# Optimization experiments

Measured on AMD Instinct MI355X. Metric: run time of the kernel, lower is better.

Reference implementation:

```python
import jax, jax.numpy as jnp
import numpy as np

H = 128          # hidden_channels == num_features for both node types
L = 3            # num_layers
E_TYPES = 3      # (a->a), (a->b), (b->a)
N = 200000       # nodes per type
E = 600000       # edges per edge type
G = 64           # graphs in batch
C = 10           # num_classes
BN_EPS = 1e-5


def setup_inputs() -> dict:
    key = jax.random.key(0)
    ks = jax.random.split(key, 16)
    x_a = jax.random.normal(ks[0], (N, H), dtype=jnp.float32)
    x_b = jax.random.normal(ks[1], (N, H), dtype=jnp.float32)
    ei_aa = jax.random.randint(ks[2], (2, E), 0, N, dtype=jnp.int32)
    ei_ab = jax.random.randint(ks[3], (2, E), 0, N, dtype=jnp.int32)
    ei_ba = jax.random.randint(ks[4], (2, E), 0, N, dtype=jnp.int32)
    batch_a = jnp.sort(jax.random.randint(ks[5], (N,), 0, G, dtype=jnp.int32))
    batch_b = jnp.sort(jax.random.randint(ks[6], (N,), 0, G, dtype=jnp.int32))
    s = 1.0 / np.sqrt(H)
    # GraphConv params per (layer, edge_type): lin_rel (weight+bias), lin_root (no bias)
    Wrel = jax.random.uniform(ks[7], (L, E_TYPES, H, H), jnp.float32, -s, s)
    brel = jax.random.uniform(ks[8], (L, E_TYPES, H), jnp.float32, -s, s)
    Wroot = jax.random.uniform(ks[9], (L, E_TYPES, H, H), jnp.float32, -s, s)
    # BatchNorm affine params per node type (0='a', 1='b')
    bn_gamma = jnp.ones((2, H), jnp.float32)
    bn_beta = jnp.zeros((2, H), jnp.float32)
    lin_W = jax.random.uniform(ks[10], (C, H), jnp.float32, -s, s)
    lin_b = jax.random.uniform(ks[11], (C,), jnp.float32, -s, s)
    return {"x_a": x_a, "x_b": x_b, "Wrel": Wrel, "brel": brel, "Wroot": Wroot,
            "bn_gamma": bn_gamma, "bn_beta": bn_beta, "lin_W": lin_W, "lin_b": lin_b,
            "ei_aa": ei_aa, "ei_ab": ei_ab, "ei_ba": ei_ba,
            "batch_a": batch_a, "batch_b": batch_b}


def _graph_conv(x_src, x_dst, ei, W_rel, b_rel, W_root):
    # PyG GraphConv (aggr='add'): out = lin_rel(sum_{j in N(i)} x_j) + lin_root(x_i)
    agg = jax.ops.segment_sum(x_src[ei[0]], ei[1], num_segments=x_dst.shape[0])
    return agg @ W_rel.T + b_rel + x_dst @ W_root.T


def _bn(x, gamma, beta):
    # BatchNorm in training mode: batch statistics (biased variance)
    mu = x.mean(axis=0)
    var = x.var(axis=0)
    return gamma * (x - mu) * jax.lax.rsqrt(var + BN_EPS) + beta


def reference(x_a, x_b, Wrel, brel, Wroot, bn_gamma, bn_beta, lin_W, lin_b,
              ei_aa, ei_ab, ei_ba, batch_a, batch_b):
    for l in range(L):
        # HeteroConv sums contributions per destination node type
        out_a = (_graph_conv(x_a, x_a, ei_aa, Wrel[l, 0], brel[l, 0], Wroot[l, 0]) +
                 _graph_conv(x_b, x_a, ei_ba, Wrel[l, 2], brel[l, 2], Wroot[l, 2]))
        out_b = _graph_conv(x_a, x_b, ei_ab, Wrel[l, 1], brel[l, 1], Wroot[l, 1])
        x_a = _bn(jax.nn.relu(out_a), bn_gamma[0], bn_beta[0])
        x_b = _bn(jax.nn.relu(out_b), bn_gamma[1], bn_beta[1])
    # global mean pool over concatenated node types
    feats = jnp.concatenate([x_a, x_b], axis=0)
    batch = jnp.concatenate([batch_a, batch_b], axis=0)
    sums = jax.ops.segment_sum(feats, batch, num_segments=G)
    counts = jax.ops.segment_sum(jnp.ones((feats.shape[0],), feats.dtype), batch, num_segments=G)
    pooled = sums / jnp.maximum(counts, 1.0)[:, None]
    return pooled @ lin_W.T + lin_b
```

## Files before the change

### kernel.cpp

```cpp
#include <hip/hip_runtime.h>
#include <hip/hip_bf16.h>

#define HF 128

typedef unsigned int uint32;
typedef unsigned short ushort16;
typedef float f32x4 __attribute__((ext_vector_type(4)));
typedef __bf16 bf16x8 __attribute__((ext_vector_type(8)));

__device__ __forceinline__ float bflo(uint32 u) { return __uint_as_float(u << 16); }
__device__ __forceinline__ float bfhi(uint32 u) { return __uint_as_float(u & 0xffff0000u); }
__device__ __forceinline__ ushort16 f2bf(float f) {
  uint32 u = __float_as_uint(f);
  return (ushort16)((u + 0x7fffu + ((u >> 16) & 1u)) >> 16);
}
__device__ __forceinline__ uint32 pack2(float lo, float hi) {
  return (uint32)f2bf(lo) | ((uint32)f2bf(hi) << 16);
}

__global__ void diag_k(float* __restrict__ out, int n, float val) {
  int i = blockIdx.x * 256 + threadIdx.x;
  if (i < n) out[i] = val;
}

__global__ __launch_bounds__(256) void setup_k(
    const float* __restrict__ xa, const float* __restrict__ xb,
    uint32* __restrict__ XA0, uint32* __restrict__ XA1, uint32* __restrict__ XB,
    int n4a, int n4b,
    int* __restrict__ cs, size_t capA, size_t capB, size_t capC, int vA, int vB,
    float* __restrict__ pool, int poolN4,
    size_t dummyA, size_t dummyB,
    int CA, int CB, int CI, int PZ) {
  int b = blockIdx.x, t = threadIdx.x;
  if (b < CA) {
    int i = b * 256 + t;
    if (i < n4a) {
      float4 v = ((const float4*)xa)[i];
      uint2 p; p.x = pack2(v.x, v.y); p.y = pack2(v.z, v.w);
      ((uint2*)XA0)[i] = p;
    }
    return;
  }
  b -= CA;
  if (b < CB) {
    int i = b * 256 + t;
    if (i < n4b) {
      float4 v = ((const float4*)xb)[i];
      uint2 p; p.x = pack2(v.x, v.y); p.y = pack2(v.z, v.w);
      ((uint2*)XB)[i] = p;
    }
    return;
  }
  b -= CB;
  if (b < CI) {
    size_t i = ((size_t)b * 256 + t) * 4;
    size_t tot = capA + capB + capC;
    if (i < tot) {
      int v = (i < capA + capB) ? vA : vB;
      int4 w = make_int4(v, v, v, v);
      *(int4*)&cs[i] = w;
    }
    return;
  }
  b -= CI;
  if (b < PZ) {
    int i = b * 256 + t;
    if (i < poolN4) ((float4*)pool)[i] = make_float4(0.f, 0.f, 0.f, 0.f);
    return;
  }
  if (t < 64) XA0[dummyA + t] = 0;
  else if (t < 128) XA1[dummyA + (t - 64)] = 0;
  else if (t < 192) XB[dummyB + (t - 128)] = 0;
}

__global__ void count3_k(const int* __restrict__ eA, int EA, int* __restrict__ rA,
                         const int* __restrict__ eB, int EB, int* __restrict__ rB,
                         const int* __restrict__ eC, int EC, int* __restrict__ rC,
                         int B0, int B1) {
  int b = blockIdx.x;
  const int* ei; int E; int* rp;
  if (b < B0)            { ei = eA; E = EA; rp = rA; }
  else if (b < B0 + B1)  { ei = eB; E = EB; rp = rB; b -= B0; }
  else                   { ei = eC; E = EC; rp = rC; b -= B0 + B1; }
  int e = b * 256 + threadIdx.x;
  if (e < E) atomicAdd(&rp[ei[E + e]], 1);
}

__device__ __forceinline__ int pad4(int c) { return (c + 3) & ~3; }

__device__ __forceinline__ void scan1_body(const int* __restrict__ rp, int N,
                                           int* __restrict__ bsum, int b, int t) {
  int i = b * 1024 + t * 4;
  int s = 0;
  if (i + 3 < N) {
    int4 v = *(const int4*)&rp[i];
    s = pad4(v.x) + pad4(v.y) + pad4(v.z) + pad4(v.w);
  } else {
    for (int j = 0; j < 4; ++j) if (i + j < N) s += pad4(rp[i + j]);
  }
  __shared__ int sd[256];
  sd[t] = s;
  __syncthreads();
  for (int o = 128; o > 0; o >>= 1) {
    if (t < o) sd[t] += sd[t + o];
    __syncthreads();
  }
  if (t == 0) bsum[b] = sd[0];
}

__global__ __launch_bounds__(256) void scan1x3_k(
    const int* __restrict__ rA, int NA, int* __restrict__ bA,
    const int* __restrict__ rB, int NB, int* __restrict__ bB,
    const int* __restrict__ rC, int NC, int* __restrict__ bC, int nbA, int nbB) {
  int b = blockIdx.x;
  if (b < nbA)            scan1_body(rA, NA, bA, b, threadIdx.x);
  else if (b < nbA + nbB) scan1_body(rB, NB, bB, b - nbA, threadIdx.x);
  else                    scan1_body(rC, NC, bC, b - nbA - nbB, threadIdx.x);
}

__global__ __launch_bounds__(1024) void scan2x3_k(int* __restrict__ bA, int nbA,
                                                  int* __restrict__ bB, int nbB,
                                                  int* __restrict__ bC, int nbC) {
  int* bsum = (blockIdx.x == 0) ? bA : (blockIdx.x == 1) ? bB : bC;
  int nb    = (blockIdx.x == 0) ? nbA : (blockIdx.x == 1) ? nbB : nbC;
  __shared__ int sd[1024];
  int t = threadIdx.x;
  int v = (t < nb) ? bsum[t] : 0;
  sd[t] = v;
  __syncthreads();
  for (int o = 1; o < 1024; o <<= 1) {
    int x = (t >= o) ? sd[t - o] : 0;
    __syncthreads();
    sd[t] += x;
    __syncthreads();
  }
  if (t < nb) bsum[t] = sd[t] - v;
}

__device__ __forceinline__ void scan3_body(int* __restrict__ rp, int* __restrict__ cur,
                                           int* __restrict__ deg,
                                           const int* __restrict__ bsum, int N,
                                           int b, int t) {
  int i = b * 1024 + t * 4;
  int c[4];
  #pragma unroll
  for (int j = 0; j < 4; ++j) c[j] = (i + j < N) ? rp[i + j] : 0;
  int tsum = pad4(c[0]) + pad4(c[1]) + pad4(c[2]) + pad4(c[3]);
  __shared__ int sd[256];
  sd[t] = tsum;
  __syncthreads();
  for (int o = 1; o < 256; o <<= 1) {
    int x = (t >= o) ? sd[t - o] : 0;
    __syncthreads();
    sd[t] += x;
    __syncthreads();
  }
  int off = bsum[b] + sd[t] - tsum;
  int p = off;
  #pragma unroll
  for (int j = 0; j < 4; ++j) {
    if (i + j < N) { rp[i + j] = p; cur[i + j] = p; deg[i + j] = c[j]; }
    p += pad4(c[j]);
  }
  if (i < N && N <= i + 4) rp[N] = off + tsum;
}

__global__ __launch_bounds__(256) void scan3x3_k(
    int* __restrict__ rA, int* __restrict__ cA, int* __restrict__ dA,
    const int* __restrict__ bA, int NA,
    int* __restrict__ rB, int* __restrict__ cB, int* __restrict__ dB,
    const int* __restrict__ bB, int NB,
    int* __restrict__ rC, int* __restrict__ cC, int* __restrict__ dC,
    const int* __restrict__ bC, int NC,
    int nbA, int nbB) {
  int b = blockIdx.x;
  if (b < nbA)            scan3_body(rA, cA, dA, bA, NA, b, threadIdx.x);
  else if (b < nbA + nbB) scan3_body(rB, cB, dB, bB, NB, b - nbA, threadIdx.x);
  else                    scan3_body(rC, cC, dC, bC, NC, b - nbA - nbB, threadIdx.x);
}

#define FILL_P 4
__global__ __launch_bounds__(256) void fill3p_k(
    const int* __restrict__ eA, int EA, int* __restrict__ cuA, int* __restrict__ csA,
    const int* __restrict__ eB, int EB, int* __restrict__ cuB, int* __restrict__ csB,
    const int* __restrict__ eC, int EC, int* __restrict__ cuC, int* __restrict__ csC,
    int NA, int NBn, int B0, int B1, int Btot) {
  int pass = blockIdx.x / Btot;
  int b = blockIdx.x % Btot;
  const int* ei; int E; int* cur; int* cs; int N;
  if (b < B0)           { ei = eA; E = EA; cur = cuA; cs = csA; N = NA; }
  else if (b < B0 + B1) { ei = eB; E = EB; cur = cuB; cs = csB; N = NBn; b -= B0; }
  else                  { ei = eC; E = EC; cur = cuC; cs = csC; N = NA; b -= B0 + B1; }
  int e = b * 256 + threadIdx.x;
  if (e >= E) return;
  int dst = ei[E + e];
  int lo = (int)(((long long)pass * N) / FILL_P);
  int hi = (int)(((long long)(pass + 1) * N) / FILL_P);
  if (dst < lo || dst >= hi) return;
  int pos = atomicAdd(&cur[dst], 1);
  cs[pos] = ei[e];
}

__global__ __launch_bounds__(128) void prep2_k(
    const float* __restrict__ Wrel_l, const float* __restrict__ Wroot_l,
    const float* __restrict__ brel_l,
    const float* __restrict__ gamma, const float* __restrict__ beta,
    const float* __restrict__ statsPrev, float* __restrict__ statsNext,
    float nA, float nB, int first,
    ushort16* __restrict__ BWa, ushort16* __restrict__ BWb,
    float* __restrict__ uvec) {
  __shared__ float red[128];
  int n = blockIdx.x, k = threadIdx.x;
  float scA, shA, scB, shB;
  if (first) {
    scA = 1.f; shA = 0.f; scB = 1.f; shB = 0.f;
  } else {
    float sA = 0.f, qA = 0.f, sB = 0.f, qB = 0.f;
    for (int st = 0; st < 64; ++st) {
      sA += statsPrev[st * 128 + k];
      qA += statsPrev[8192 + st * 128 + k];
      sB += statsPrev[16384 + st * 128 + k];
      qB += statsPrev[24576 + st * 128 + k];
    }
    float mA = sA / nA, vA = qA / nA - mA * mA;
    float rA = rsqrtf(vA + 1e-5f);
    scA = gamma[k] * rA; shA = beta[k] - mA * scA;
    float mB = sB / nB, vB = qB / nB - mB * mB;
    float rB = rsqrtf(vB + 1e-5f);
    scB = gamma[128 + k] * rB; shB = beta[128 + k] - mB * scB;
  }
  if (n < 64) {
    float4 z = make_float4(0.f, 0.f, 0.f, 0.f);
    *(float4*)&statsNext[n * 512 + k * 4] = z;
  }
  float w0  = Wrel_l[n * HF + k];
  float w1  = Wrel_l[16384 + n * HF + k];
  float w2  = Wrel_l[32768 + n * HF + k];
  float wr1 = Wroot_l[16384 + n * HF + k];
  float wrc = Wroot_l[n * HF + k] + Wroot_l[32768 + n * HF + k];

  int ksl = k >> 5;
  int lane = (n & 15) + (((k >> 3) & 3) << 4);
  int j = k & 7;
  int nt = n >> 4;
  auto put = [&](ushort16* B, int ksb, float v) {
    B[((size_t)((ksb + ksl) * 8 + nt) * 64 + lane) * 8 + j] = f2bf(v);
  };
  put(BWa, 0, scA * w0);
  put(BWa, 4, scB * w2);
  put(BWa, 8, scA * wrc);
  put(BWb, 0, scA * w1);
  put(BWb, 4, scB * wr1);

  auto reduce = [&](float v) -> float {
    red[k] = v;
    __syncthreads();
    for (int s = 64; s > 0; s >>= 1) {
      if (k < s) red[k] += red[k + s];
      __syncthreads();
    }
    float r = red[0];
    __syncthreads();
    return r;
  };
  float r0 = reduce(shA * w0);
  float r1 = reduce(shB * w2);
  float r2 = reduce(shA * w1);
  float r3 = reduce(shA * wrc);
  float r4 = reduce(shB * wr1);
  if (k == 0) {
    uvec[n]       = r0;
    uvec[128 + n] = r1;
    uvec[256 + n] = r2;
    uvec[384 + n] = brel_l[n] + brel_l[256 + n] + r3;
    uvec[512 + n] = brel_l[128 + n] + r4;
  }
}

template <bool HAS2>
__global__ __launch_bounds__(256) void gg_k(
    const uint32* __restrict__ Xg1, const int* __restrict__ rp1, const int* __restrict__ cs1,
    const int* __restrict__ deg1,
    const uint32* __restrict__ Xg2, const int* __restrict__ rp2, const int* __restrict__ cs2,
    const int* __restrict__ deg2,
    const uint32* Xr,
    const bf16x8* __restrict__ BW,
    const float* __restrict__ u1, const float* __restrict__ u2,
    const float* __restrict__ bias,
    uint32* out,
    float* __restrict__ statS, float* __restrict__ statQ,
    int nRows) {
  constexpr int KS_G = HAS2 ? 8 : 4;
  __shared__ uint32 lds[4][1088];
  int tid = threadIdx.x, wid = tid >> 6, l = tid & 63;
  int R0 = blockIdx.x * 64 + wid * 16;
  uint32* L = &lds[wid][0];
  int row = l & 15, khi = l >> 4;
  int myRow = R0 + row;
  bool okRow = myRow < nRows;
  int rowIdx = okRow ? myRow : nRows;

  int e0a = 0, e1a = 0;
  if (okRow) { e0a = rp1[myRow]; e1a = rp1[myRow + 1]; }
  int e0b = 0, e1b = 0;
  if constexpr (HAS2) { if (okRow) { e0b = rp2[myRow]; e1b = rp2[myRow + 1]; } }
  bf16x8 rt[4];
  #pragma unroll
  for (int ks = 0; ks < 4; ++ks)
    rt[ks] = *(const bf16x8*)&Xr[(size_t)rowIdx * 64 + (ks * 4 + khi) * 4];
  int4 q1 = make_int4(0, 0, 0, 0), q2 = make_int4(0, 0, 0, 0);
  if (e0a < e1a) q1 = *(const int4*)&cs1[e0a];
  if constexpr (HAS2) { if (e0b < e1b) q2 = *(const int4*)&cs2[e0b]; }
  int rl0 = khi * 4;
  float dg1[4] = {0.f, 0.f, 0.f, 0.f}, dg2[4] = {0.f, 0.f, 0.f, 0.f};
  #pragma unroll
  for (int j = 0; j < 4; ++j) {
    int r = R0 + rl0 + j;
    if (r < nRows) {
      dg1[j] = (float)deg1[r];
      if constexpr (HAS2) dg2[j] = (float)deg2[r];
    }
  }

  float lo[16], hi[16];
  auto addv = [&](int base, uint4 v) {
    hi[base + 0] += __uint_as_float(v.x); lo[base + 0] += __uint_as_float(v.x << 16);
    hi[base + 1] += __uint_as_float(v.y); lo[base + 1] += __uint_as_float(v.y << 16);
    hi[base + 2] += __uint_as_float(v.z); lo[base + 2] += __uint_as_float(v.z << 16);
    hi[base + 3] += __uint_as_float(v.w); lo[base + 3] += __uint_as_float(v.w << 16);
  };
  auto run_tile = [&](const uint32* __restrict__ Xg, const int* __restrict__ cs,
                      int e0, int e1, int4 qinit) {
    #pragma unroll
    for (int i = 0; i < 16; ++i) { lo[i] = 0.f; hi[i] = 0.f; }
    if (e0 >= e1) return;
    int e = e0;
    int4 q = qinit;
    for (;;) {
      const uint32* p0 = &Xg[(size_t)q.x * 64 + khi * 4];
      const uint32* p1 = &Xg[(size_t)q.y * 64 + khi * 4];
      const uint32* p2 = &Xg[(size_t)q.z * 64 + khi * 4];
      const uint32* p3 = &Xg[(size_t)q.w * 64 + khi * 4];
      uint4 a0 = *(const uint4*)&p0[0];
      uint4 a1 = *(const uint4*)&p0[16];
      uint4 a2 = *(const uint4*)&p0[32];
      uint4 a3 = *(const uint4*)&p0[48];
      uint4 b0 = *(const uint4*)&p1[0];
      uint4 b1 = *(const uint4*)&p1[16];
      uint4 b2 = *(const uint4*)&p1[32];
      uint4 b3 = *(const uint4*)&p1[48];
      uint4 c0 = *(const uint4*)&p2[0];
      uint4 c1 = *(const uint4*)&p2[16];
      uint4 c2 = *(const uint4*)&p2[32];
      uint4 c3 = *(const uint4*)&p2[48];
      uint4 d0 = *(const uint4*)&p3[0];
      uint4 d1 = *(const uint4*)&p3[16];
      uint4 d2 = *(const uint4*)&p3[32];
      uint4 d3 = *(const uint4*)&p3[48];
      int en = e + 4;
      bool more = en < e1;
      int4 qn = q;
      if (more) qn = *(const int4*)&cs[en];
      addv(0, a0); addv(4, a1); addv(8, a2); addv(12, a3);
      addv(0, b0); addv(4, b1); addv(8, b2); addv(12, b3);
      addv(0, c0); addv(4, c1); addv(8, c2); addv(12, c3);
      addv(0, d0); addv(4, d1); addv(8, d2); addv(12, d3);
      if (!more) break;
      e = en; q = qn;
    }
  };
  auto to_frag = [&](int ks) -> bf16x8 {
    bf16x8 a;
    #pragma unroll
    for (int j = 0; j < 4; ++j) {
      a[2 * j]     = (__bf16)lo[ks * 4 + j];
      a[2 * j + 1] = (__bf16)hi[ks * 4 + j];
    }
    return a;
  };

  run_tile(Xg1, cs1, e0a, e1a, q1);
  bf16x8 af1[4];
  #pragma unroll
  for (int ks = 0; ks < 4; ++ks) af1[ks] = to_frag(ks);

  bf16x8 af2[4];
  if constexpr (HAS2) {
    run_tile(Xg2, cs2, e0b, e1b, q2);
    #pragma unroll
    for (int ks = 0; ks < 4; ++ks) af2[ks] = to_frag(ks);
  }

  f32x4 acc[8] = {};
  const bf16x8* Bl = BW + l;
  #pragma unroll
  for (int ks = 0; ks < 4; ++ks) {
    #pragma unroll
    for (int nt = 0; nt < 8; ++nt) {
      bf16x8 b = Bl[(size_t)(ks * 8 + nt) * 64];
      acc[nt] = __builtin_amdgcn_mfma_f32_16x16x32_bf16(af1[ks], b, acc[nt], 0, 0, 0);
    }
  }
  if constexpr (HAS2) {
    #pragma unroll
    for (int ks = 0; ks < 4; ++ks) {
      #pragma unroll
      for (int nt = 0; nt < 8; ++nt) {
        bf16x8 b = Bl[(size_t)((4 + ks) * 8 + nt) * 64];
        acc[nt] = __builtin_amdgcn_mfma_f32_16x16x32_bf16(af2[ks], b, acc[nt], 0, 0, 0);
      }
    }
  }
  #pragma unroll
  for (int ks = 0; ks < 4; ++ks) {
    #pragma unroll
    for (int nt = 0; nt < 8; ++nt) {
      bf16x8 b = Bl[(size_t)((KS_G + ks) * 8 + nt) * 64];
      acc[nt] = __builtin_amdgcn_mfma_f32_16x16x32_bf16(rt[ks], b, acc[nt], 0, 0, 0);
    }
  }

  ushort16* P = (ushort16*)L;
  int c0 = l & 15;
  float ps[8], pq[8];
  #pragma unroll
  for (int nt = 0; nt < 8; ++nt) {
    int col = nt * 16 + c0;
    float bc = bias[col];
    float u1c = u1[col];
    float u2c = HAS2 ? u2[col] : 0.f;
    float s = 0.f, q = 0.f;
    #pragma unroll
    for (int j = 0; j < 4; ++j) {
      float v = acc[nt][j] + bc + dg1[j] * u1c;
      if constexpr (HAS2) v += dg2[j] * u2c;
      v = fmaxf(v, 0.f);
      if (R0 + rl0 + j < nRows) { s += v; q += v * v; }
      P[(rl0 + j) * 136 + col] = f2bf(v);
    }
    ps[nt] = s; pq[nt] = q;
  }

  #pragma unroll
  for (int rr = 0; rr < 4; ++rr) {
    int rloc = rr * 4 + khi;
    int grow = R0 + rloc;
    if (grow < nRows) {
      uint4 v = *(const uint4*)&P[rloc * 136 + c0 * 8];
      *(uint4*)&out[(size_t)grow * 64 + c0 * 4] = v;
    }
  }

  #pragma unroll
  for (int nt = 0; nt < 8; ++nt) {
    ps[nt] += __shfl_xor(ps[nt], 16); ps[nt] += __shfl_xor(ps[nt], 32);
    pq[nt] += __shfl_xor(pq[nt], 16); pq[nt] += __shfl_xor(pq[nt], 32);
  }
  if (l < 16) {
    float* S = statS + (size_t)(blockIdx.x & 63) * 128;
    float* Q = statQ + (size_t)(blockIdx.x & 63) * 128;
    #pragma unroll
    for (int nt = 0; nt < 8; ++nt) {
      unsafeAtomicAdd(&S[nt * 16 + l], ps[nt]);
      unsafeAtomicAdd(&Q[nt * 16 + l], pq[nt]);
    }
  }
}

__global__ void bn_fin_k(const float* __restrict__ stats, const float* __restrict__ gamma,
                         const float* __restrict__ beta, float* __restrict__ ss,
                         float nA, float nB) {
  int t = threadIdx.x;
  if (t >= 256) return;
  int type = t >> 7, f = t & 127;
  const float* S = stats + (size_t)type * 16384;
  const float* Q = S + 8192;
  float s = 0.f, q = 0.f;
  for (int st = 0; st < 64; ++st) { s += S[st * 128 + f]; q += Q[st * 128 + f]; }
  float nN = type ? nB : nA;
  float mean = s / nN;
  float var = q / nN - mean * mean;
  float rstd = rsqrtf(var + 1e-5f);
  float sc = gamma[type * HF + f] * rstd;
  float sh = beta[type * HF + f] - mean * sc;
  ss[type * 256 + f] = sc;
  ss[type * 256 + 128 + f] = sh;
}

__global__ __launch_bounds__(256) void pool_k(const uint32* __restrict__ x,
                                              const int* __restrict__ batch,
                                              const float* __restrict__ scale,
                                              const float* __restrict__ shift,
                                              float* __restrict__ pool, int nN) {
  int f2 = threadIdx.x & 31;
  int sub = threadIdx.x >> 5;
  int start = blockIdx.x * 1024;
  int end = min(start + 1024, nN);
  float4 sc = *(const float4*)&scale[f2 * 4];
  float4 sh = *(const float4*)&shift[f2 * 4];
  float a0 = 0.f, a1 = 0.f, a2 = 0.f, a3 = 0.f, cnt = 0.f;
  int cur = -1;
  for (int n = start + sub; n < end; n += 8) {
    int g = batch[n];
    if (g != cur) {
      if (cur >= 0) {
        float* bp = &pool[(size_t)cur * HF + f2 * 4];
        unsafeAtomicAdd(bp + 0, sc.x * a0 + cnt * sh.x);
        unsafeAtomicAdd(bp + 1, sc.y * a1 + cnt * sh.y);
        unsafeAtomicAdd(bp + 2, sc.z * a2 + cnt * sh.z);
        unsafeAtomicAdd(bp + 3, sc.w * a3 + cnt * sh.w);
      }
      a0 = a1 = a2 = a3 = 0.f; cnt = 0.f; cur = g;
    }
    uint2 v = *(const uint2*)&x[(size_t)n * 64 + f2 * 2];
    a0 += bflo(v.x); a1 += bfhi(v.x); a2 += bflo(v.y); a3 += bfhi(v.y);
    cnt += 1.f;
  }
  if (cur >= 0) {
    float* bp = &pool[(size_t)cur * HF + f2 * 4];
    unsafeAtomicAdd(bp + 0, sc.x * a0 + cnt * sh.x);
    unsafeAtomicAdd(bp + 1, sc.y * a1 + cnt * sh.y);
    unsafeAtomicAdd(bp + 2, sc.z * a2 + cnt * sh.z);
    unsafeAtomicAdd(bp + 3, sc.w * a3 + cnt * sh.w);
  }
}

__device__ inline int lowerb(const int* a, int n, int v) {
  int lo = 0, hi = n;
  while (lo < hi) { int m = (lo + hi) >> 1; if (a[m] < v) lo = m + 1; else hi = m; }
  return lo;
}

__global__ void final_k(const float* __restrict__ pool,
                        const int* __restrict__ ba, int nA,
                        const int* __restrict__ bb, int nB,
                        const float* __restrict__ linW, const float* __restrict__ linb,
                        float* __restrict__ out, int Cn) {
  int g = blockIdx.x;
  int lane = threadIdx.x;
  int c = (lowerb(ba, nA, g + 1) - lowerb(ba, nA, g)) +
          (lowerb(bb, nB, g + 1) - lowerb(bb, nB, g));
  float inv = 1.f / fmaxf((float)c, 1.f);
  float p0 = pool[(size_t)g * HF + lane] * inv;
  float p1 = pool[(size_t)g * HF + 64 + lane] * inv;
  for (int cc = 0; cc < Cn; ++cc) {
    float t = p0 * linW[cc * HF + lane] + p1 * linW[cc * HF + 64 + lane];
    for (int off = 32; off > 0; off >>= 1) t += __shfl_down(t, off);
    if (lane == 0) out[g * Cn + cc] = t + linb[cc];
  }
}

extern "C" void kernel_launch(void* const* d_in, const int* in_sizes, int n_in,
                              void* d_out, int out_size, void* d_ws, size_t ws_size,
                              hipStream_t stream) {
  const float* x_a   = (const float*)d_in[0];
  const float* x_b   = (const float*)d_in[1];
  const float* Wrel  = (const float*)d_in[2];
  const float* brel  = (const float*)d_in[3];
  const float* Wroot = (const float*)d_in[4];
  const float* bn_g  = (const float*)d_in[5];
  const float* bn_b  = (const float*)d_in[6];
  const float* lin_W = (const float*)d_in[7];
  const float* lin_b = (const float*)d_in[8];
  const int* ei_aa   = (const int*)d_in[9];
  const int* ei_ab   = (const int*)d_in[10];
  const int* ei_ba   = (const int*)d_in[11];
  const int* batch_a = (const int*)d_in[12];
  const int* batch_b = (const int*)d_in[13];

  int Na  = in_sizes[0] / HF;
  int Nb  = in_sizes[1] / HF;
  int Eaa = in_sizes[9] / 2;
  int Eab = in_sizes[10] / 2;
  int Eba = in_sizes[11] / 2;
  int Cn  = in_sizes[7] / HF;
  int Gn  = out_size / Cn;

  size_t NHa = (size_t)Na * HF, NHb = (size_t)Nb * HF;
  size_t capA = ((size_t)Eaa + 3 * (size_t)Na + 15) & ~(size_t)15;
  size_t capB = ((size_t)Eab + 3 * (size_t)Nb + 15) & ~(size_t)15;
  size_t capC = ((size_t)Eba + 3 * (size_t)Na + 15) & ~(size_t)15;

  char* base = (char*)d_ws;
  auto alignup = [](size_t x) { return (x + 255) & ~(size_t)255; };
  size_t off = 0;
  size_t oXA0 = off; off = alignup(off + (NHa + HF) * 2);
  size_t oXA1 = off; off = alignup(off + (NHa + HF) * 2);
  size_t oXB  = off; off = alignup(off + (NHb + HF) * 2);
  size_t oRP  = off; off = alignup(off + ((size_t)(Na + 1) + (Nb + 1) + (Na + 1)) * 4);
  size_t oCUR = off; off = alignup(off + ((size_t)Na + Nb + Na) * 4);
  size_t oDEG = off; off = alignup(off + ((size_t)Na + Nb + Na) * 4);
  size_t oCS  = off; off = alignup(off + (capA + capB + capC) * 4);
  size_t oBWA = off; off = alignup(off + (size_t)12 * 8 * 64 * 16);
  size_t oBWB = off; off = alignup(off + (size_t)8 * 8 * 64 * 16);
  size_t oUV  = off; off = alignup(off + 5 * 128 * 4);
  size_t oSS  = off; off = alignup(off + 512 * 4);
  size_t oST  = off; off = alignup(off + 65536 * 4);
  size_t oBS  = off; off = alignup(off + 3072 * 4);
  size_t oPOOL= off; off = alignup(off + (size_t)Gn * HF * 4);
  size_t need = off;

  if (ws_size < need) {
    diag_k<<<(out_size + 255) / 256, 256, 0, stream>>>(
        (float*)d_out, out_size, (float)((double)ws_size / 1048576.0));
    return;
  }

  uint32* XA0 = (uint32*)(base + oXA0);
  uint32* XA1 = (uint32*)(base + oXA1);
  uint32* XB  = (uint32*)(base + oXB);
  int* rp_aa = (int*)(base + oRP);
  int* rp_ab = rp_aa + (Na + 1);
  int* rp_ba = rp_ab + (Nb + 1);
  int* cur_aa = (int*)(base + oCUR);
  int* cur_ab = cur_aa + Na;
  int* cur_ba = cur_ab + Nb;
  int* deg_aa = (int*)(base + oDEG);
  int* deg_ab = deg_aa + Na;
  int* deg_ba = deg_ab + Nb;
  int* cs_aa = (int*)(base + oCS);
  int* cs_ab = cs_aa + capA;
  int* cs_ba = cs_ab + capB;
  ushort16* BWa = (ushort16*)(base + oBWA);
  ushort16* BWb = (ushort16*)(base + oBWB);
  float* uvec  = (float*)(base + oUV);
  float* ss    = (float*)(base + oSS);
  float* stats = (float*)(base + oST);
  int* bsum    = (int*)(base + oBS);
  float* pool  = (float*)(base + oPOOL);

  float* ss_a = ss;
  float* ss_b = ss + 256;
  float* uaa = uvec, *uba = uvec + 128, *uab = uvec + 256;
  float* bias_a = uvec + 384, *bias_b = uvec + 512;

  int n4a = (int)(NHa / 4), n4b = (int)(NHb / 4);
  int CA = (n4a + 255) / 256, CB = (n4b + 255) / 256;
  size_t capTot = capA + capB + capC;
  int CI = (int)((capTot / 4 + 255) / 256);
  int poolN4 = Gn * HF / 4;
  int PZ = (poolN4 + 255) / 256;
  setup_k<<<CA + CB + CI + PZ + 1, 256, 0, stream>>>(
      x_a, x_b, XA0, XA1, XB, n4a, n4b,
      cs_aa, capA, capB, capC, Na, Nb,
      pool, poolN4, NHa / 2, NHb / 2, CA, CB, CI, PZ);

  hipMemsetAsync(rp_aa, 0, ((size_t)(Na + 1) + (Nb + 1) + (Na + 1)) * 4, stream);
  int B0 = (Eaa + 255) / 256, B1 = (Eab + 255) / 256, B2 = (Eba + 255) / 256;
  count3_k<<<B0 + B1 + B2, 256, 0, stream>>>(ei_aa, Eaa, rp_aa, ei_ab, Eab, rp_ab,
                                             ei_ba, Eba, rp_ba, B0, B1);

  int nb_a = (Na + 1023) / 1024;
  int nb_b = (Nb + 1023) / 1024;
  scan1x3_k<<<nb_a + nb_b + nb_a, 256, 0, stream>>>(
      rp_aa, Na, bsum, rp_ab, Nb, bsum + 1024, rp_ba, Na, bsum + 2048, nb_a, nb_b);
  scan2x3_k<<<3, 1024, 0, stream>>>(bsum, nb_a, bsum + 1024, nb_b, bsum + 2048, nb_a);
  scan3x3_k<<<nb_a + nb_b + nb_a, 256, 0, stream>>>(
      rp_aa, cur_aa, deg_aa, bsum, Na,
      rp_ab, cur_ab, deg_ab, bsum + 1024, Nb,
      rp_ba, cur_ba, deg_ba, bsum + 2048, Na, nb_a, nb_b);

  int Btot = B0 + B1 + B2;
  fill3p_k<<<FILL_P * Btot, 256, 0, stream>>>(ei_aa, Eaa, cur_aa, cs_aa,
                                              ei_ab, Eab, cur_ab, cs_ab,
                                              ei_ba, Eba, cur_ba, cs_ba,
                                              Na, Nb, B0, B1, Btot);

  uint32* xa_cur = XA0;
  uint32* xa_nxt = XA1;
  for (int l = 0; l < 3; ++l) {
    const float* Wrel_l  = Wrel  + (size_t)l * 3 * 16384;
    const float* Wroot_l = Wroot + (size_t)l * 3 * 16384;
    const float* brel_l  = brel  + (size_t)l * 3 * HF;
    float* statsCur  = stats + (size_t)(l & 1) * 32768;
    float* statsPrev = stats + (size_t)((l + 1) & 1) * 32768;

    prep2_k<<<128, 128, 0, stream>>>(Wrel_l, Wroot_l, brel_l, bn_g, bn_b,
                                     statsPrev, statsCur, (float)Na, (float)Nb,
                                     (l == 0) ? 1 : 0, BWa, BWb, uvec);

    gg_k<true><<<(Na + 63) / 64, 256, 0, stream>>>(
        xa_cur, rp_aa, cs_aa, deg_aa, XB, rp_ba, cs_ba, deg_ba, xa_cur,
        (const bf16x8*)BWa, uaa, uba, bias_a, xa_nxt,
        statsCur, statsCur + 8192, Na);
    gg_k<false><<<(Nb + 63) / 64, 256, 0, stream>>>(
        xa_cur, rp_ab, cs_ab, deg_ab, nullptr, nullptr, nullptr, nullptr, XB,
        (const bf16x8*)BWb, uab, nullptr, bias_b, XB,
        statsCur + 16384, statsCur + 24576, Nb);

    uint32* t = xa_cur; xa_cur = xa_nxt; xa_nxt = t;
  }

  bn_fin_k<<<1, 256, 0, stream>>>(stats, bn_g, bn_b, ss, (float)Na, (float)Nb);

  pool_k<<<(Na + 1023) / 1024, 256, 0, stream>>>(xa_cur, batch_a, ss_a, ss_a + 128, pool, Na);
  pool_k<<<(Nb + 1023) / 1024, 256, 0, stream>>>(XB, batch_b, ss_b, ss_b + 128, pool, Nb);
  final_k<<<Gn, 64, 0, stream>>>(pool, batch_a, Na, batch_b, Nb,
                                 lin_W, lin_b, (float*)d_out, Cn);
}
```

Before: 969.4 us.

## Merge per-layer a/b GraphConv kernels into one launch with double-buffered XB

```diff
diff --git a/kernel.cpp b/kernel.cpp
--- a/kernel.cpp
+++ b/kernel.cpp
@@ -25,12 +25,14 @@
 
 __global__ __launch_bounds__(256) void setup_k(
     const float* __restrict__ xa, const float* __restrict__ xb,
-    uint32* __restrict__ XA0, uint32* __restrict__ XA1, uint32* __restrict__ XB,
+    uint32* __restrict__ XA0, uint32* __restrict__ XA1,
+    uint32* __restrict__ XB0, uint32* __restrict__ XB1,
     int n4a, int n4b,
     int* __restrict__ cs, size_t capA, size_t capB, size_t capC, int vA, int vB,
     float* __restrict__ pool, int poolN4,
+    int* __restrict__ rpz, int rpN4,
     size_t dummyA, size_t dummyB,
-    int CA, int CB, int CI, int PZ) {
+    int CA, int CB, int CI, int PZ, int RZ) {
   int b = blockIdx.x, t = threadIdx.x;
   if (b < CA) {
     int i = b * 256 + t;
@@ -47,7 +49,7 @@
     if (i < n4b) {
       float4 v = ((const float4*)xb)[i];
       uint2 p; p.x = pack2(v.x, v.y); p.y = pack2(v.z, v.w);
-      ((uint2*)XB)[i] = p;
+      ((uint2*)XB0)[i] = p;
     }
     return;
   }
@@ -68,9 +70,16 @@
     if (i < poolN4) ((float4*)pool)[i] = make_float4(0.f, 0.f, 0.f, 0.f);
     return;
   }
+  b -= PZ;
+  if (b < RZ) {
+    int i = b * 256 + t;
+    if (i < rpN4) ((int4*)rpz)[i] = make_int4(0, 0, 0, 0);
+    return;
+  }
   if (t < 64) XA0[dummyA + t] = 0;
   else if (t < 128) XA1[dummyA + (t - 64)] = 0;
-  else if (t < 192) XB[dummyB + (t - 128)] = 0;
+  else if (t < 192) XB0[dummyB + (t - 128)] = 0;
+  else XB1[dummyB + (t - 192)] = 0;
 }
 
 __global__ void count3_k(const int* __restrict__ eA, int EA, int* __restrict__ rA,
@@ -278,7 +287,8 @@
 }
 
 template <bool HAS2>
-__global__ __launch_bounds__(256) void gg_k(
+__device__ __forceinline__ void gg_body(
+    int blk,
     const uint32* __restrict__ Xg1, const int* __restrict__ rp1, const int* __restrict__ cs1,
     const int* __restrict__ deg1,
     const uint32* __restrict__ Xg2, const int* __restrict__ rp2, const int* __restrict__ cs2,
@@ -289,12 +299,10 @@
     const float* __restrict__ bias,
     uint32* out,
     float* __restrict__ statS, float* __restrict__ statQ,
-    int nRows) {
+    int nRows, uint32* L) {
   constexpr int KS_G = HAS2 ? 8 : 4;
-  __shared__ uint32 lds[4][1088];
-  int tid = threadIdx.x, wid = tid >> 6, l = tid & 63;
-  int R0 = blockIdx.x * 64 + wid * 16;
-  uint32* L = &lds[wid][0];
+  int tid = threadIdx.x, l = tid & 63, wid = tid >> 6;
+  int R0 = blk * 64 + wid * 16;
   int row = l & 15, khi = l >> 4;
   int myRow = R0 + row;
   bool okRow = myRow < nRows;
@@ -457,13 +465,38 @@
     pq[nt] += __shfl_xor(pq[nt], 16); pq[nt] += __shfl_xor(pq[nt], 32);
   }
   if (l < 16) {
-    float* S = statS + (size_t)(blockIdx.x & 63) * 128;
-    float* Q = statQ + (size_t)(blockIdx.x & 63) * 128;
+    float* S = statS + (size_t)(blk & 63) * 128;
+    float* Q = statQ + (size_t)(blk & 63) * 128;
     #pragma unroll
     for (int nt = 0; nt < 8; ++nt) {
       unsafeAtomicAdd(&S[nt * 16 + l], ps[nt]);
       unsafeAtomicAdd(&Q[nt * 16 + l], pq[nt]);
     }
+  }
+}
+
+__global__ __launch_bounds__(256) void gg2_k(
+    const uint32* __restrict__ XAc, const uint32* __restrict__ XBc,
+    const int* __restrict__ rp_aa, const int* __restrict__ cs_aa, const int* __restrict__ deg_aa,
+    const int* __restrict__ rp_ba, const int* __restrict__ cs_ba, const int* __restrict__ deg_ba,
+    const int* __restrict__ rp_ab, const int* __restrict__ cs_ab, const int* __restrict__ deg_ab,
+    const bf16x8* __restrict__ BWa, const bf16x8* __restrict__ BWb,
+    const float* __restrict__ uvec,
+    uint32* outA, uint32* outB,
+    float* __restrict__ stats,
+    int Na, int Nb, int nbA) {
+  __shared__ uint32 lds[4][1088];
+  uint32* L = &lds[threadIdx.x >> 6][0];
+  int b = blockIdx.x;
+  if (b < nbA) {
+    gg_body<true>(b, XAc, rp_aa, cs_aa, deg_aa, XBc, rp_ba, cs_ba, deg_ba,
+                  XAc, BWa, uvec, uvec + 128, uvec + 384, outA,
+                  stats, stats + 8192, Na, L);
+  } else {
+    gg_body<false>(b - nbA, XAc, rp_ab, cs_ab, deg_ab,
+                   nullptr, nullptr, nullptr, nullptr,
+                   XBc, BWb, uvec + 256, nullptr, uvec + 512, outB,
+                   stats + 16384, stats + 24576, Nb, L);
   }
 }
 
@@ -586,7 +619,7 @@
   size_t off = 0;
   size_t oXA0 = off; off = alignup(off + (NHa + HF) * 2);
   size_t oXA1 = off; off = alignup(off + (NHa + HF) * 2);
-  size_t oXB  = off; off = alignup(off + (NHb + HF) * 2);
+  size_t oXB0 = off; off = alignup(off + (NHb + HF) * 2);
   size_t oRP  = off; off = alignup(off + ((size_t)(Na + 1) + (Nb + 1) + (Na + 1)) * 4);
   size_t oCUR = off; off = alignup(off + ((size_t)Na + Nb + Na) * 4);
   size_t oDEG = off; off = alignup(off + ((size_t)Na + Nb + Na) * 4);
@@ -598,17 +631,21 @@
   size_t oST  = off; off = alignup(off + 65536 * 4);
   size_t oBS  = off; off = alignup(off + 3072 * 4);
   size_t oPOOL= off; off = alignup(off + (size_t)Gn * HF * 4);
-  size_t need = off;
-
-  if (ws_size < need) {
+  size_t need_min = off;
+  size_t oXB1 = off; off = alignup(off + (NHb + HF) * 2);
+  size_t need_full = off;
+
+  if (ws_size < need_min) {
     diag_k<<<(out_size + 255) / 256, 256, 0, stream>>>(
         (float*)d_out, out_size, (float)((double)ws_size / 1048576.0));
     return;
   }
+  bool merged = ws_size >= need_full;
 
   uint32* XA0 = (uint32*)(base + oXA0);
   uint32* XA1 = (uint32*)(base + oXA1);
-  uint32* XB  = (uint32*)(base + oXB);
+  uint32* XB0 = (uint32*)(base + oXB0);
+  uint32* XB1 = merged ? (uint32*)(base + oXB1) : XB0;
   int* rp_aa = (int*)(base + oRP);
   int* rp_ab = rp_aa + (Na + 1);
   int* rp_ba = rp_ab + (Nb + 1);
@@ -631,8 +668,6 @@
 
   float* ss_a = ss;
   float* ss_b = ss + 256;
-  float* uaa = uvec, *uba = uvec + 128, *uab = uvec + 256;
-  float* bias_a = uvec + 384, *bias_b = uvec + 512;
 
   int n4a = (int)(NHa / 4), n4b = (int)(NHb / 4);
   int CA = (n4a + 255) / 256, CB = (n4b + 255) / 256;
@@ -640,12 +675,15 @@
   int CI = (int)((capTot / 4 + 255) / 256);
   int poolN4 = Gn * HF / 4;
   int PZ = (poolN4 + 255) / 256;
-  setup_k<<<CA + CB + CI + PZ + 1, 256, 0, stream>>>(
-      x_a, x_b, XA0, XA1, XB, n4a, n4b,
+  int rpCnt = (Na + 1) + (Nb + 1) + (Na + 1);
+  int rpN4 = (rpCnt + 3) / 4;
+  int RZ = (rpN4 + 255) / 256;
+  setup_k<<<CA + CB + CI + PZ + RZ + 1, 256, 0, stream>>>(
+      x_a, x_b, XA0, XA1, XB0, XB1, n4a, n4b,
       cs_aa, capA, capB, capC, Na, Nb,
-      pool, poolN4, NHa / 2, NHb / 2, CA, CB, CI, PZ);
-
-  hipMemsetAsync(rp_aa, 0, ((size_t)(Na + 1) + (Nb + 1) + (Na + 1)) * 4, stream);
+      pool, poolN4, rp_aa, rpN4,
+      NHa / 2, NHb / 2, CA, CB, CI, PZ, RZ);
+
   int B0 = (Eaa + 255) / 256, B1 = (Eab + 255) / 256, B2 = (Eba + 255) / 256;
   count3_k<<<B0 + B1 + B2, 256, 0, stream>>>(ei_aa, Eaa, rp_aa, ei_ab, Eab, rp_ab,
                                              ei_ba, Eba, rp_ba, B0, B1);
@@ -666,8 +704,12 @@
                                               ei_ba, Eba, cur_ba, cs_ba,
                                               Na, Nb, B0, B1, Btot);
 
+  int nbA = (Na + 63) / 64;
+  int nbB = (Nb + 63) / 64;
   uint32* xa_cur = XA0;
   uint32* xa_nxt = XA1;
+  uint32* xb_cur = XB0;
+  uint32* xb_nxt = XB1;
   for (int l = 0; l < 3; ++l) {
     const float* Wrel_l  = Wrel  + (size_t)l * 3 * 16384;
     const float* Wroot_l = Wroot + (size_t)l * 3 * 16384;
@@ -679,22 +721,32 @@
                                      statsPrev, statsCur, (float)Na, (float)Nb,
                                      (l == 0) ? 1 : 0, BWa, BWb, uvec);
 
-    gg_k<true><<<(Na + 63) / 64, 256, 0, stream>>>(
-        xa_cur, rp_aa, cs_aa, deg_aa, XB, rp_ba, cs_ba, deg_ba, xa_cur,
-        (const bf16x8*)BWa, uaa, uba, bias_a, xa_nxt,
-        statsCur, statsCur + 8192, Na);
-    gg_k<false><<<(Nb + 63) / 64, 256, 0, stream>>>(
-        xa_cur, rp_ab, cs_ab, deg_ab, nullptr, nullptr, nullptr, nullptr, XB,
-        (const bf16x8*)BWb, uab, nullptr, bias_b, XB,
-        statsCur + 16384, statsCur + 24576, Nb);
-
+    if (merged) {
+      gg2_k<<<nbA + nbB, 256, 0, stream>>>(
+          xa_cur, xb_cur, rp_aa, cs_aa, deg_aa, rp_ba, cs_ba, deg_ba,
+          rp_ab, cs_ab, deg_ab,
+          (const bf16x8*)BWa, (const bf16x8*)BWb, uvec,
+          xa_nxt, xb_nxt, statsCur, Na, Nb, nbA);
+      uint32* t2 = xb_cur; xb_cur = xb_nxt; xb_nxt = t2;
+    } else {
+      gg2_k<<<nbA, 256, 0, stream>>>(
+          xa_cur, xb_cur, rp_aa, cs_aa, deg_aa, rp_ba, cs_ba, deg_ba,
+          rp_ab, cs_ab, deg_ab,
+          (const bf16x8*)BWa, (const bf16x8*)BWb, uvec,
+          xa_nxt, nullptr, statsCur, Na, Nb, nbA);
+      gg2_k<<<nbB, 256, 0, stream>>>(
+          xa_cur, xb_cur, rp_aa, cs_aa, deg_aa, rp_ba, cs_ba, deg_ba,
+          rp_ab, cs_ab, deg_ab,
+          (const bf16x8*)BWa, (const bf16x8*)BWb, uvec,
+          nullptr, xb_cur, statsCur, Na, Nb, 0);
+    }
     uint32* t = xa_cur; xa_cur = xa_nxt; xa_nxt = t;
   }
 
   bn_fin_k<<<1, 256, 0, stream>>>(stats, bn_g, bn_b, ss, (float)Na, (float)Nb);
 
   pool_k<<<(Na + 1023) / 1024, 256, 0, stream>>>(xa_cur, batch_a, ss_a, ss_a + 128, pool, Na);
-  pool_k<<<(Nb + 1023) / 1024, 256, 0, stream>>>(XB, batch_b, ss_b, ss_b + 128, pool, Nb);
+  pool_k<<<(Nb + 1023) / 1024, 256, 0, stream>>>(xb_cur, batch_b, ss_b, ss_b + 128, pool, Nb);
   final_k<<<Gn, 64, 0, stream>>>(pool, batch_a, Na, batch_b, Nb,
                                  lin_W, lin_b, (float*)d_out, Cn);
 }
```

Measured after the change: 927.0 us (median of 2 runs). 1.05x faster.
